# Kernel tuning notes

Hardware: AMD Instinct MI355X
Metric: run time of the kernel (lower is better)

## Reference

```python
import jax, jax.numpy as jnp
import numpy as np

VOXEL_SIZE = 0.05  # init kwarg


def setup_inputs() -> dict:
    key = jax.random.key(0)
    N, B = 4_194_304, 16
    # coords uniform in [0, 5)^3 -> ~100^3 voxel cells per scene at voxel_size=0.05
    coord = jax.random.uniform(key, (N, 3), dtype=jnp.float32) * 5.0
    # cumulative batch offsets (equal-sized scenes), as pointops expects
    offset = (jnp.arange(1, B + 1, dtype=jnp.int32) * (N // B)).astype(jnp.int32)
    return {"coord": coord, "offset": offset}


def _voxel_mean(coord, offset, voxel_size):
    """Faithful jax port of voxelize_helper + segment_csr(mean) + batch2offset.

    Returns:
      n_p    [N,3]  voxel-mean coords, padded with zeros beyond n_voxels
      n_o    [B]    cumulative voxel counts per batch (batch2offset)
      counts [N]    points per voxel (idx_ptr = concat([0], cumsum(counts[valid])))
    """
    N = coord.shape[0]
    B = offset.shape[0]
    # batch id per point from cumulative offsets
    batch = jnp.searchsorted(offset, jnp.arange(N), side='right')  # [N]
    # start = per-batch min coord (start=None path of voxelize_helper)
    start = jax.ops.segment_min(coord, batch, num_segments=B)      # [B,3]
    grid = jnp.floor((coord - start[batch]) / voxel_size).astype(jnp.int32)  # [N,3]
    G = jnp.max(grid) + 1  # grid extent (per-axis upper bound)
    # linearized cluster key: unique per (batch, gx, gy, gz)
    ckey = ((batch * G + grid[:, 0]) * G + grid[:, 1]) * G + grid[:, 2]
    fill = B * G * G * G  # sentinel beyond any real key
    # sorted unique cluster keys == CSR segment order after sorting cluster indices
    uniq, inv = jnp.unique(ckey, return_inverse=True, size=N, fill_value=fill)
    # fused gather + segment-mean (equivalent to coord[sorted_idx] -> segment_csr mean)
    seg_sum = jax.ops.segment_sum(coord, inv, num_segments=N)                 # [N,3]
    counts = jax.ops.segment_sum(jnp.ones((N,), coord.dtype), inv, num_segments=N)
    n_p = seg_sum / jnp.maximum(counts, 1.0)[:, None]
    # batch id per voxel -> batch2offset (cumulative voxel counts)
    valid = uniq < fill
    vbatch = jnp.where(valid, uniq // (G * G * G), B)
    per_batch = jax.ops.segment_sum(valid.astype(jnp.int32), vbatch, num_segments=B + 1)[:B]
    n_o = jnp.cumsum(per_batch)
    return n_p, n_o, counts.astype(jnp.int32)


def reference(coord, offset):
    return _voxel_mean(coord, offset, VOXEL_SIZE)
```

## Files before the change

### kernel.cpp

```cpp
#include <hip/hip_runtime.h>
#include <stdint.h>


typedef unsigned int uint;
typedef unsigned long long u64;

#define VS 0.05f
#define QSCALE (4096.0f / VS)
#define QINV  (VS / 4096.0f)
#define NBUCKET 2048
#define NBLK_P 256
#define DENSE_MAX 4096

__device__ __forceinline__ uint f2m(float f) {
    uint b = __float_as_uint(f);
    return (b & 0x80000000u) ? ~b : (b | 0x80000000u);
}
__device__ __forceinline__ float m2f(uint m) {
    uint b = (m & 0x80000000u) ? (m & 0x7fffffffu) : ~m;
    return __uint_as_float(b);
}

__global__ void k_init(uint* start_m, int B3) {
    int i = blockIdx.x * blockDim.x + threadIdx.x;
    if (i < B3) start_m[i] = 0xFFFFFFFFu;
}

__global__ void __launch_bounds__(256)
k_minmax(const float* __restrict__ coord, const int* __restrict__ offset,
         int N, int B, uint* start_m) {
    __shared__ uint smin[768];
    __shared__ int soff[256];
    int t = threadIdx.x;
    int nb3 = B * 3;
    for (int j = t; j < B; j += 256) soff[j] = offset[j];
    for (int j = t; j < nb3; j += 256) smin[j] = 0xFFFFFFFFu;
    __syncthreads();

    int F = 3 * N;
    int NQ = F >> 2;
    int per = (NQ + gridDim.x - 1) / gridDim.x;
    int qlo = blockIdx.x * per;
    int qhi = min(NQ, qlo + per);
    const float4* __restrict__ c4 = reinterpret_cast<const float4*>(coord);

    bool fast = false;
    int bU = 0;
    if (qlo < qhi) {
        int pF = (4 * qlo) / 3;
        int pL = (4 * qhi - 1) / 3;
        int bF = 0, bL = 0;
        for (int j = 0; j < B; ++j) {
            bF += (pF >= soff[j]) ? 1 : 0;
            bL += (pL >= soff[j]) ? 1 : 0;
        }
        fast = (bF == bL);
        bU = bF;
    }

    if (fast) {
        int q = qlo + t;
        int p0 = q % 3;
        float s0 = INFINITY, s1 = INFINITY, s2 = INFINITY;
        for (;;) {
            if (q >= qhi) break;
            float4 v = c4[q];
            s0 = fminf(s0, fminf(v.x, v.w)); s1 = fminf(s1, v.y); s2 = fminf(s2, v.z);
            q += 256;
            if (q >= qhi) break;
            v = c4[q];
            s1 = fminf(s1, fminf(v.x, v.w)); s2 = fminf(s2, v.y); s0 = fminf(s0, v.z);
            q += 256;
            if (q >= qhi) break;
            v = c4[q];
            s2 = fminf(s2, fminf(v.x, v.w)); s0 = fminf(s0, v.y); s1 = fminf(s1, v.z);
            q += 256;
        }
        float ax, ay, az;
        if (p0 == 0)      { ax = s0; ay = s1; az = s2; }
        else if (p0 == 1) { ax = s2; ay = s0; az = s1; }
        else              { ax = s1; ay = s2; az = s0; }
        for (int d = 32; d; d >>= 1) {
            ax = fminf(ax, __shfl_xor(ax, d));
            ay = fminf(ay, __shfl_xor(ay, d));
            az = fminf(az, __shfl_xor(az, d));
        }
        if ((t & 63) == 0 && ax < INFINITY) {
            atomicMin(&smin[bU * 3 + 0], f2m(ax));
            atomicMin(&smin[bU * 3 + 1], f2m(ay));
            atomicMin(&smin[bU * 3 + 2], f2m(az));
        }
    } else {
        for (int q = qlo + t; q < qhi; q += 256) {
            float4 v = c4[q];
            int e = 4 * q;
            float vals[4] = {v.x, v.y, v.z, v.w};
#pragma unroll
            for (int k = 0; k < 4; ++k) {
                int ee = e + k;
                int pt = ee / 3;
                int axis = ee - 3 * pt;
                int b = 0;
                for (int j = 0; j < B; ++j) b += (pt >= soff[j]) ? 1 : 0;
                atomicMin(&smin[b * 3 + axis], f2m(vals[k]));
            }
        }
    }

    if (blockIdx.x == 0) {
        for (int ee = 4 * NQ + t; ee < F; ee += 256) {
            int pt = ee / 3;
            int axis = ee - 3 * pt;
            int b = 0;
            for (int j = 0; j < B; ++j) b += (pt >= soff[j]) ? 1 : 0;
            atomicMin(&smin[b * 3 + axis], f2m(coord[ee]));
        }
    }
    __syncthreads();
    for (int j = t; j < nb3; j += 256) {
        uint mn = smin[j];
        if (mn != 0xFFFFFFFFu) atomicMin(&start_m[j], mn);
    }
}


__device__ __forceinline__ u64 mk_rec(float x, float y, float z,
                                      float sx, float sy, float sz,
                                      int b, uint& q) {
    int gx = min((int)floorf((x - sx) / VS), 127);
    int gy = min((int)floorf((y - sy) / VS), 127);
    int gz = min((int)floorf((z - sz) / VS), 127);
    float fx = fmaxf(x - (sx + (float)gx * VS), 0.0f);
    float fy = fmaxf(y - (sy + (float)gy * VS), 0.0f);
    float fz = fmaxf(z - (sz + (float)gz * VS), 0.0f);
    uint ux = min((uint)(fx * QSCALE + 0.5f), 4095u);
    uint uy = min((uint)(fy * QSCALE + 0.5f), 4095u);
    uint uz = min((uint)(fz * QSCALE + 0.5f), 4095u);
    uint cell = ((uint)gy << 7) | (uint)gz;
    q = ((uint)b << 7) | (uint)gx;
    return ((u64)q << 50) | ((u64)cell << 36) | ((u64)ux << 24) | ((u64)uy << 12) | (u64)uz;
}

__device__ __forceinline__ void count_point(float x, float y, float z, int b,
                                            float sx, float sy, float sz, int pid,
                                            uint* hist, u64* __restrict__ tmp) {
    uint q;
    u64 rec = mk_rec(x, y, z, sx, sy, sz, b, q);
    atomicAdd(&hist[q], 1u);
    tmp[pid] = rec;
}

__global__ void __launch_bounds__(1024)
k_count3(const float* __restrict__ coord, const int* __restrict__ offset,
         int N, int B, const uint* __restrict__ start_m, uint* __restrict__ histm,
         u64* __restrict__ tmp) {
    __shared__ uint hist[NBUCKET];
    __shared__ int soff[16];
    __shared__ float sstart[48];
    int t = threadIdx.x;
    if (t < B) soff[t] = offset[t];
    if (t < B * 3) sstart[t] = m2f(start_m[t]);
    for (int j = t; j < NBUCKET; j += 1024) hist[j] = 0;
    __syncthreads();
    int chunk = (N + gridDim.x - 1) / gridDim.x;
    int lo = blockIdx.x * chunk, hi = min(N, lo + chunk);
    int bLo = 0, bHi = 0;
    for (int j = 0; j < B; ++j) {
        bLo += (lo >= soff[j]) ? 1 : 0;
        bHi += (hi - 1 >= soff[j]) ? 1 : 0;
    }
    if (lo < hi && bLo == bHi && (lo & 3) == 0) {
        int b = bLo;
        float sx = sstart[b * 3 + 0], sy = sstart[b * 3 + 1], sz = sstart[b * 3 + 2];
        const float4* __restrict__ c4 = reinterpret_cast<const float4*>(coord);
        int gEnd = hi >> 2;
        for (int g = (lo >> 2) + t; g < gEnd; g += 1024) {
            float4 v0 = c4[3 * g], v1 = c4[3 * g + 1], v2 = c4[3 * g + 2];
            int p = 4 * g;
            count_point(v0.x, v0.y, v0.z, b, sx, sy, sz, p + 0, hist, tmp);
            count_point(v0.w, v1.x, v1.y, b, sx, sy, sz, p + 1, hist, tmp);
            count_point(v1.z, v1.w, v2.x, b, sx, sy, sz, p + 2, hist, tmp);
            count_point(v2.y, v2.z, v2.w, b, sx, sy, sz, p + 3, hist, tmp);
        }
        for (int i = (gEnd << 2) + t; i < hi; i += 1024) {
            float x = coord[3 * i + 0], y = coord[3 * i + 1], z = coord[3 * i + 2];
            count_point(x, y, z, b, sx, sy, sz, i, hist, tmp);
        }
    } else {
        for (int i = lo + t; i < hi; i += 1024) {
            float x = coord[3 * i + 0], y = coord[3 * i + 1], z = coord[3 * i + 2];
            int b = 0;
            for (int j = 0; j < B; ++j) b += (i >= soff[j]) ? 1 : 0;
            count_point(x, y, z, b, sstart[b * 3 + 0], sstart[b * 3 + 1],
                        sstart[b * 3 + 2], i, hist, tmp);
        }
    }
    __syncthreads();
    for (int j = t; j < NBUCKET; j += 1024)
        histm[(size_t)j * NBLK_P + blockIdx.x] = hist[j];
}

__global__ void __launch_bounds__(256)
k_scanrow(uint* __restrict__ histm, uint* __restrict__ tot) {
    __shared__ uint wtot[4], woff[4];
    uint* row = histm + (size_t)blockIdx.x * NBLK_P;
    int t = threadIdx.x;
    uint v = row[t];
    uint sc = v;
    for (int d = 1; d < 64; d <<= 1) {
        uint nb = __shfl_up(sc, d, 64);
        if ((t & 63) >= d) sc += nb;
    }
    if ((t & 63) == 63) wtot[t >> 6] = sc;
    __syncthreads();
    if (t == 0) {
        uint r = 0;
#pragma unroll
        for (int k = 0; k < 4; ++k) { woff[k] = r; r += wtot[k]; }
    }
    __syncthreads();
    uint incl = sc + woff[t >> 6];
    row[t] = incl - v;
    if (t == 255) tot[blockIdx.x] = incl;
}

__global__ void __launch_bounds__(1024)
k_scan2048(const uint* __restrict__ in, uint* __restrict__ out) {
    __shared__ uint wtot[16], woff[16];
    int t = threadIdx.x;
    uint a = in[2 * t], bb = in[2 * t + 1];
    uint s = a + bb;
    uint sc = s;
    for (int d = 1; d < 64; d <<= 1) {
        uint nb = __shfl_up(sc, d, 64);
        if ((t & 63) >= d) sc += nb;
    }
    if ((t & 63) == 63) wtot[t >> 6] = sc;
    __syncthreads();
    if (t == 0) {
        uint r = 0;
#pragma unroll
        for (int k = 0; k < 16; ++k) { woff[k] = r; r += wtot[k]; }
    }
    __syncthreads();
    uint incl = sc + woff[t >> 6];
    uint ex = incl - s;
    out[2 * t] = ex;
    out[2 * t + 1] = ex + a;
    if (t == 1023) out[2048] = incl;
}

__global__ void __launch_bounds__(1024)
k_scan2048b(const uint* __restrict__ in, uint* __restrict__ out,
            int B, float* __restrict__ no_out) {
    __shared__ uint wtot[16], woff[16];
    int t = threadIdx.x;
    uint a = in[2 * t], bb = in[2 * t + 1];
    uint s = a + bb;
    uint sc = s;
    for (int d = 1; d < 64; d <<= 1) {
        uint nb = __shfl_up(sc, d, 64);
        if ((t & 63) >= d) sc += nb;
    }
    if ((t & 63) == 63) wtot[t >> 6] = sc;
    __syncthreads();
    if (t == 0) {
        uint r = 0;
#pragma unroll
        for (int k = 0; k < 16; ++k) { woff[k] = r; r += wtot[k]; }
    }
    __syncthreads();
    uint incl = sc + woff[t >> 6];
    uint ex = incl - s;
    out[2 * t] = ex;
    out[2 * t + 1] = ex + a;
    if (t == 1023) out[2048] = incl;
    int tp = t + 1;
    if ((tp & 63) == 0) {
        int b = (tp >> 6) - 1;
        if (b < B) no_out[b] = (float)incl;
    }
}

__global__ void __launch_bounds__(1024)
k_scatter(const u64* __restrict__ tmp, int N,
          const uint* __restrict__ histm, const uint* __restrict__ bucket_base,
          u64* __restrict__ recs) {
    __shared__ uint cursor[NBUCKET];
    int t = threadIdx.x;
    for (int j = t; j < NBUCKET; j += 1024)
        cursor[j] = bucket_base[j] + histm[(size_t)j * NBLK_P + blockIdx.x];
    __syncthreads();
    int chunk = (N + gridDim.x - 1) / gridDim.x;
    int lo = blockIdx.x * chunk, hi = min(N, lo + chunk);
    for (int i = lo + t; i < hi; i += 1024) {
        u64 r = tmp[i];
        uint q = (uint)(r >> 50);
        uint slot = atomicAdd(&cursor[q], 1u);
        recs[slot] = r;
    }
}

__global__ void k_vox(const u64* __restrict__ recs, const uint* __restrict__ bucket_base,
                      uint* __restrict__ voxcount, uint* __restrict__ gmask) {
    __shared__ uint bits[512];
    __shared__ uint wsum[4];
    int q = blockIdx.x;
    uint lo = bucket_base[q], hi = bucket_base[q + 1];
    for (int j = threadIdx.x; j < 512; j += blockDim.x) bits[j] = 0;
    __syncthreads();
    for (uint i = lo + threadIdx.x; i < hi; i += blockDim.x) {
        uint c = (uint)(recs[i] >> 36) & 0x3FFFu;
        atomicOr(&bits[c >> 5], 1u << (c & 31));
    }
    __syncthreads();
    uint s = 0;
    for (int w = threadIdx.x; w < 512; w += blockDim.x) {
        uint m = bits[w];
        gmask[(size_t)q * 512 + w] = m;
        s += __popc(m);
    }
    for (int d = 32; d; d >>= 1) s += __shfl_xor(s, d);
    if ((threadIdx.x & 63) == 0) wsum[threadIdx.x >> 6] = s;
    __syncthreads();
    if (threadIdx.x == 0) voxcount[q] = wsum[0] + wsum[1] + wsum[2] + wsum[3];
}

__global__ void __launch_bounds__(512)
k_emit2(const u64* __restrict__ recs, const uint* __restrict__ bucket_base,
        const uint* __restrict__ voxscan, const uint* __restrict__ gmask,
        const uint* __restrict__ start_m, int N, int B, int out_total,
        float* __restrict__ np_out, float* __restrict__ cnt_out,
        float* __restrict__ out) {
    int t = threadIdx.x;
    if (blockIdx.x >= NBUCKET) {
        uint total = voxscan[NBUCKET];
        int zb = blockIdx.x - NBUCKET;
        int stride = (gridDim.x - NBUCKET) * 512;
        int tid = zb * 512 + t;
        for (int j = 3 * (int)total + tid; j < 3 * N; j += stride) np_out[j] = 0.0f;
        for (int j = (int)total + tid; j < N; j += stride) cnt_out[j] = 0.0f;
        for (int j = 4 * N + B + tid; j < out_total; j += stride) out[j] = 0.0f;
        return;
    }
    __shared__ u64 dense[DENSE_MAX];
    __shared__ uint mask[512], wrank[512];
    __shared__ uint wtot[8], woff[9];
    __shared__ float sstart[48];
    int q = blockIdx.x;
    uint lo = bucket_base[q], hi = bucket_base[q + 1];
    if (lo == hi) return;
    if (t < 48) sstart[t] = m2f(start_m[t]);
    uint m = gmask[(size_t)q * 512 + t];
    mask[t] = m;
    uint c = __popc(m);
    uint sc = c;
    for (int d = 1; d < 64; d <<= 1) {
        uint nb = __shfl_up(sc, d, 64);
        if ((t & 63) >= d) sc += nb;
    }
    if ((t & 63) == 63) wtot[t >> 6] = sc;
    __syncthreads();
    if (t == 0) {
        uint r = 0;
#pragma unroll
        for (int k = 0; k < 8; ++k) { woff[k] = r; r += wtot[k]; }
        woff[8] = r;
    }
    __syncthreads();
    wrank[t] = sc - c + woff[t >> 6];
    uint vc = woff[8];
    uint base_r = voxscan[q];
    int b = q >> 7, gx = q & 127;
    float cx = sstart[b * 3 + 0] + (float)gx * VS;
    float sy = sstart[b * 3 + 1], sz = sstart[b * 3 + 2];
    bool single = (vc <= (uint)DENSE_MAX);
    for (uint segbase = 0; segbase < vc; segbase += DENSE_MAX) {
        uint seglen = min(vc - segbase, (uint)DENSE_MAX);
        for (uint j = t; j < seglen; j += 512) dense[j] = 0ull;
        __syncthreads();
        if (single) {
            for (uint i = lo + t; i < hi; i += 512) {
                u64 rec = recs[i];
                uint cc = (uint)(rec >> 36) & 0x3FFFu;
                uint w = cc >> 5, bit = cc & 31;
                uint r = wrank[w] + __popc(mask[w] & ((1u << bit) - 1u));
                u64 enc = (((rec >> 24) & 0xFFFull) << 46) | (((rec >> 12) & 0xFFFull) << 28)
                        | ((rec & 0xFFFull) << 10) | 1ull;
                atomicAdd(&dense[r], enc);
            }
        } else {
            for (uint i = lo + t; i < hi; i += 512) {
                u64 rec = recs[i];
                uint cc = (uint)(rec >> 36) & 0x3FFFu;
                uint w = cc >> 5, bit = cc & 31;
                uint r = wrank[w] + __popc(mask[w] & ((1u << bit) - 1u));
                if (r >= segbase && r < segbase + seglen) {
                    u64 enc = (((rec >> 24) & 0xFFFull) << 46) | (((rec >> 12) & 0xFFFull) << 28)
                            | ((rec & 0xFFFull) << 10) | 1ull;
                    atomicAdd(&dense[r - segbase], enc);
                }
            }
        }
        __syncthreads();
        {
            uint mm = mask[t];
            uint r = wrank[t];
            uint kbase = (uint)t << 5;
            while (mm) {
                uint bit = (uint)__ffs(mm) - 1u;
                mm &= mm - 1u;
                if (r >= segbase && r < segbase + seglen) {
                    uint cell = kbase + bit;
                    uint gy = cell >> 7, gz = cell & 127u;
                    u64 p = dense[r - segbase];
                    float cnt = (float)(uint)(p & 1023ull);
                    float inv = 1.0f / fmaxf(cnt, 1.0f);
                    uint uz = (uint)((p >> 10) & 0x3FFFFull);
                    uint uy = (uint)((p >> 28) & 0x3FFFFull);
                    uint ux = (uint)(p >> 46);
                    uint r_out = base_r + r;
                    np_out[3 * r_out + 0] = cx + ((float)ux * QINV) * inv;
                    np_out[3 * r_out + 1] = sy + (float)gy * VS + ((float)uy * QINV) * inv;
                    np_out[3 * r_out + 2] = sz + (float)gz * VS + ((float)uz * QINV) * inv;
                    cnt_out[r_out] = cnt;
                }
                ++r;
            }
        }
        __syncthreads();
    }
}


__device__ __forceinline__ void point_grid(const float* __restrict__ coord, int i,
                                           const int* soff, const float* sstart, int B,
                                           float& x, float& y, float& z,
                                           int& b, int& gx, int& gy, int& gz) {
    x = coord[3 * i + 0]; y = coord[3 * i + 1]; z = coord[3 * i + 2];
    b = 0;
    for (int j = 0; j < B; ++j) b += (i >= soff[j]) ? 1 : 0;
    gx = min((int)floorf((x - sstart[b * 3 + 0]) / VS), 127);
    gy = min((int)floorf((y - sstart[b * 3 + 1]) / VS), 127);
    gz = min((int)floorf((z - sstart[b * 3 + 2]) / VS), 127);
}

__device__ __forceinline__ u64 frac12(float x, float y, float z,
                                      const float* sstart, int b,
                                      int gx, int gy, int gz) {
    float fx = fmaxf(x - (sstart[b * 3 + 0] + (float)gx * VS), 0.0f);
    float fy = fmaxf(y - (sstart[b * 3 + 1] + (float)gy * VS), 0.0f);
    float fz = fmaxf(z - (sstart[b * 3 + 2] + (float)gz * VS), 0.0f);
    uint ux = min((uint)(fx * QSCALE + 0.5f), 4095u);
    uint uy = min((uint)(fy * QSCALE + 0.5f), 4095u);
    uint uz = min((uint)(fz * QSCALE + 0.5f), 4095u);
    return ((u64)ux << 24) | ((u64)uy << 12) | (u64)uz;
}

__global__ void k_hist(const float* __restrict__ coord, const int* __restrict__ offset,
                       int N, int B, const uint* __restrict__ start_m,
                       uint* __restrict__ mask) {
    __shared__ int soff[256];
    __shared__ float sstart[768];
    for (int j = threadIdx.x; j < B; j += blockDim.x) soff[j] = offset[j];
    for (int j = threadIdx.x; j < B * 3; j += blockDim.x) sstart[j] = m2f(start_m[j]);
    __syncthreads();
    int i = blockIdx.x * blockDim.x + threadIdx.x;
    if (i >= N) return;
    float x, y, z; int b, gx, gy, gz;
    point_grid(coord, i, soff, sstart, B, x, y, z, b, gx, gy, gz);
    uint key = ((uint)b << 21) | ((uint)gx << 14) | ((uint)gy << 7) | (uint)gz;
    atomicOr(&mask[key >> 5], 1u << (key & 31));
}

__global__ void k_scan1(const uint* __restrict__ mask, uint* __restrict__ partial) {
    int base = blockIdx.x * 1024 + threadIdx.x * 4;
    uint4 m = *(const uint4*)(mask + base);
    uint s = __popc(m.x) + __popc(m.y) + __popc(m.z) + __popc(m.w);
    for (int d = 32; d; d >>= 1) s += __shfl_xor(s, d);
    __shared__ uint wsum[4];
    if ((threadIdx.x & 63) == 0) wsum[threadIdx.x >> 6] = s;
    __syncthreads();
    if (threadIdx.x == 0) partial[blockIdx.x] = wsum[0] + wsum[1] + wsum[2] + wsum[3];
}

__global__ void k_scan2(uint* partial, int P, uint* total) {
    __shared__ uint t[256];
    uint carry = 0;
    for (int base = 0; base < P; base += 256) {
        int j = base + threadIdx.x;
        uint v = (j < P) ? partial[j] : 0;
        t[threadIdx.x] = v;
        __syncthreads();
        for (int d = 1; d < 256; d <<= 1) {
            uint add = (threadIdx.x >= d) ? t[threadIdx.x - d] : 0;
            __syncthreads();
            t[threadIdx.x] += add;
            __syncthreads();
        }
        uint inc = t[threadIdx.x];
        uint chunk = t[255];
        if (j < P) partial[j] = carry + inc - v;
        __syncthreads();
        carry += chunk;
    }
    if (threadIdx.x == 0) *total = carry;
}

__global__ void k_scan3(const uint* __restrict__ mask, const uint* __restrict__ partial,
                        uint* __restrict__ wordrank) {
    int base = blockIdx.x * 1024 + threadIdx.x * 4;
    uint4 m = *(const uint4*)(mask + base);
    uint c0 = __popc(m.x), c1 = __popc(m.y), c2 = __popc(m.z), c3 = __popc(m.w);
    uint s = c0 + c1 + c2 + c3;
    __shared__ uint t[256];
    t[threadIdx.x] = s;
    __syncthreads();
    for (int d = 1; d < 256; d <<= 1) {
        uint add = (threadIdx.x >= d) ? t[threadIdx.x - d] : 0;
        __syncthreads();
        t[threadIdx.x] += add;
        __syncthreads();
    }
    uint ex = t[threadIdx.x] - s + partial[blockIdx.x];
    uint4 r;
    r.x = ex; r.y = ex + c0; r.z = ex + c0 + c1; r.w = ex + c0 + c1 + c2;
    *(uint4*)(wordrank + base) = r;
}

__global__ void k_no(const uint* mask, const uint* wordrank, const uint* total,
                     float* no_out, int B, int W) {
    int b = blockIdx.x * blockDim.x + threadIdx.x;
    if (b >= B) return;
    long long idx = (long long)(b + 1) << 21;
    uint w = (uint)(idx >> 5);
    uint v;
    if (w >= (uint)W) v = *total;
    else v = wordrank[w];
    no_out[b] = (float)v;
}

__global__ void k_accum_sparse(const float* __restrict__ coord, const int* __restrict__ offset,
                               int N, int B, const uint* __restrict__ start_m,
                               const uint* __restrict__ mask, const uint* __restrict__ wordrank,
                               u64* __restrict__ packed) {
    __shared__ int soff[256];
    __shared__ float sstart[768];
    for (int j = threadIdx.x; j < B; j += blockDim.x) soff[j] = offset[j];
    for (int j = threadIdx.x; j < B * 3; j += blockDim.x) sstart[j] = m2f(start_m[j]);
    __syncthreads();
    int i = blockIdx.x * blockDim.x + threadIdx.x;
    if (i >= N) return;
    float x, y, z; int b, gx, gy, gz;
    point_grid(coord, i, soff, sstart, B, x, y, z, b, gx, gy, gz);
    uint key = ((uint)b << 21) | ((uint)gx << 14) | ((uint)gy << 7) | (uint)gz;
    uint w = key >> 5, bit = key & 31;
    uint r = wordrank[w] + __popc(mask[w] & ((1u << bit) - 1u));
    u64 f = frac12(x, y, z, sstart, b, gx, gy, gz);
    u64 enc = (((f >> 24) & 0xFFFull) << 46) | (((f >> 12) & 0xFFFull) << 28)
            | ((f & 0xFFFull) << 10) | 1ull;
    atomicAdd(&packed[r], enc);
}

__global__ void k_decode_sparse(const uint* __restrict__ mask, const uint* __restrict__ wordrank,
                                const uint* __restrict__ start_m,
                                const u64* __restrict__ packed, int W,
                                float* __restrict__ np_out, float* __restrict__ cnt_out) {
    __shared__ float sstart[48];
    for (int j = threadIdx.x; j < 48; j += blockDim.x) sstart[j] = m2f(start_m[j]);
    __syncthreads();
    int w = blockIdx.x * blockDim.x + threadIdx.x;
    if (w >= W) return;
    uint m = mask[w];
    if (m == 0) return;
    uint r = wordrank[w];
    uint kbase = (uint)w << 5;
    while (m) {
        uint bit = (uint)__ffs(m) - 1u;
        m &= m - 1u;
        uint key = kbase + bit;
        u64 p = packed[r];
        float cnt = (float)(uint)(p & 1023ull);
        float inv = 1.0f / fmaxf(cnt, 1.0f);
        uint uz = (uint)((p >> 10) & 0x3FFFFull);
        uint uy = (uint)((p >> 28) & 0x3FFFFull);
        uint ux = (uint)(p >> 46);
        uint b = key >> 21;
        uint gx = (key >> 14) & 127u;
        uint gy = (key >> 7) & 127u;
        uint gz = key & 127u;
        np_out[3 * r + 0] = sstart[b * 3 + 0] + (float)gx * VS + ((float)ux * QINV) * inv;
        np_out[3 * r + 1] = sstart[b * 3 + 1] + (float)gy * VS + ((float)uy * QINV) * inv;
        np_out[3 * r + 2] = sstart[b * 3 + 2] + (float)gz * VS + ((float)uz * QINV) * inv;
        cnt_out[r] = cnt;
        ++r;
    }
}

extern "C" void kernel_launch(void* const* d_in, const int* in_sizes, int n_in,
                              void* d_out, int out_size, void* d_ws, size_t ws_size,
                              hipStream_t stream) {
    const float* coord = (const float*)d_in[0];
    const int* offset = (const int*)d_in[1];
    int N = in_sizes[0] / 3;
    int B = in_sizes[1];

    float* out = (float*)d_out;
    float* np_out = out;
    float* no_out = out + (size_t)3 * N;
    float* cnt_out = no_out + B;

    uint8_t* base = (uint8_t*)d_ws;
    uint* start_m = (uint*)base;
    uint* total = start_m + (size_t)B * 3;

    uintptr_t p = (uintptr_t)(total + 1);
    p = (p + 255) & ~(uintptr_t)255;
    uint* histm = (uint*)p;          p += (size_t)NBUCKET * NBLK_P * 4;
    p = (p + 255) & ~(uintptr_t)255;
    uint* tot = (uint*)p;            p += (size_t)NBUCKET * 4;
    p = (p + 255) & ~(uintptr_t)255;
    uint* bucket_base = (uint*)p;    p += (size_t)(NBUCKET + 1) * 4;
    p = (p + 255) & ~(uintptr_t)255;
    uint* voxcount = (uint*)p;       p += (size_t)NBUCKET * 4;
    p = (p + 255) & ~(uintptr_t)255;
    uint* voxscan = (uint*)p;        p += (size_t)(NBUCKET + 1) * 4;
    p = (p + 255) & ~(uintptr_t)255;
    uint* gmask = (uint*)p;          p += (size_t)NBUCKET * 512 * 4;
    p = (p + 255) & ~(uintptr_t)255;
    u64* recs = (u64*)p;             p += (size_t)N * 8;
    p = (p + 255) & ~(uintptr_t)255;
    u64* tmp = (u64*)p;              p += (size_t)N * 8;
    size_t need_part = p - (uintptr_t)base;

    k_init<<<(B * 3 + 255) / 256, 256, 0, stream>>>(start_m, B * 3);
    k_minmax<<<2048, 256, 0, stream>>>(coord, offset, N, B, start_m);

    if (B <= 16 && ws_size >= need_part) {
        k_count3<<<NBLK_P, 1024, 0, stream>>>(coord, offset, N, B, start_m, histm, tmp);
        k_scanrow<<<NBUCKET, 256, 0, stream>>>(histm, tot);
        k_scan2048<<<1, 1024, 0, stream>>>(tot, bucket_base);
        k_scatter<<<NBLK_P, 1024, 0, stream>>>(tmp, N, histm, bucket_base, recs);
        k_vox<<<NBUCKET, 256, 0, stream>>>(recs, bucket_base, voxcount, gmask);
        k_scan2048b<<<1, 1024, 0, stream>>>(voxcount, voxscan, B, no_out);
        k_emit2<<<NBUCKET + 1024, 512, 0, stream>>>(recs, bucket_base, voxscan, gmask,
                                                    start_m, N, B, out_size,
                                                    np_out, cnt_out, out);
    } else {
        hipMemsetAsync(d_out, 0, (size_t)out_size * sizeof(float), stream);
        size_t W = (size_t)B << 16;
        int nblk1 = (int)(W / 1024);
        uintptr_t sp = (uintptr_t)(total + 1);
        sp = (sp + 255) & ~(uintptr_t)255;
        uint* partial = (uint*)sp;   sp += (size_t)nblk1 * 4;
        sp = (sp + 255) & ~(uintptr_t)255;
        uint* mask = (uint*)sp;      sp += W * 4;
        sp = (sp + 255) & ~(uintptr_t)255;
        uint* wordrank = (uint*)sp;  sp += W * 4;
        sp = (sp + 255) & ~(uintptr_t)255;
        u64* packed = (u64*)sp;
        int nb = (N + 255) / 256;
        hipMemsetAsync(mask, 0, W * sizeof(uint), stream);
        hipMemsetAsync(packed, 0, (size_t)N * sizeof(u64), stream);
        k_hist<<<nb, 256, 0, stream>>>(coord, offset, N, B, start_m, mask);
        k_scan1<<<nblk1, 256, 0, stream>>>(mask, partial);
        k_scan2<<<1, 256, 0, stream>>>(partial, nblk1, total);
        k_scan3<<<nblk1, 256, 0, stream>>>(mask, partial, wordrank);
        k_no<<<(B + 63) / 64, 64, 0, stream>>>(mask, wordrank, total, no_out, B, (int)W);
        k_accum_sparse<<<nb, 256, 0, stream>>>(coord, offset, N, B, start_m, mask,
                                               wordrank, packed);
        k_decode_sparse<<<(int)((W + 255) / 256), 256, 0, stream>>>(mask, wordrank, start_m,
                                                                    packed, (int)W,
                                                                    np_out, cnt_out);
    }
}
```

Before: 237.9 us.

## Widen emit kernel to 1024 threads and emit voxels via rank-indexed cell table

The emit kernel now runs 1024 threads per bucket. Before accumulation, each mask-word thread records the cell index for each voxel rank in a shared u16 table. Output is then written by iterating ranks contiguously across all threads, instead of having each mask-word thread walk its own bits serially. The aim is to remove the serial, divergent per-word output loop and to get coalesced output writes. The cost is extra shared memory and a larger block, which may reduce occupancy. k_vox is also simplified to fixed 256-thread indexing.

Measured after the change: 194.1 us (median of 2 runs). 1.23x faster.

```diff
diff --git a/kernel.cpp b/kernel.cpp
--- a/kernel.cpp
+++ b/kernel.cpp
@@ -3,6 +3,7 @@
 
 
 typedef unsigned int uint;
+typedef unsigned short u16;
 typedef unsigned long long u64;
 
 #define VS 0.05f
@@ -301,32 +302,33 @@
     }
 }
 
-__global__ void k_vox(const u64* __restrict__ recs, const uint* __restrict__ bucket_base,
-                      uint* __restrict__ voxcount, uint* __restrict__ gmask) {
+__global__ void __launch_bounds__(256)
+k_vox(const u64* __restrict__ recs, const uint* __restrict__ bucket_base,
+      uint* __restrict__ voxcount, uint* __restrict__ gmask) {
     __shared__ uint bits[512];
     __shared__ uint wsum[4];
     int q = blockIdx.x;
+    int t = threadIdx.x;
     uint lo = bucket_base[q], hi = bucket_base[q + 1];
-    for (int j = threadIdx.x; j < 512; j += blockDim.x) bits[j] = 0;
-    __syncthreads();
-    for (uint i = lo + threadIdx.x; i < hi; i += blockDim.x) {
+    bits[t] = 0;
+    bits[t + 256] = 0;
+    __syncthreads();
+    for (uint i = lo + t; i < hi; i += 256) {
         uint c = (uint)(recs[i] >> 36) & 0x3FFFu;
         atomicOr(&bits[c >> 5], 1u << (c & 31));
     }
     __syncthreads();
-    uint s = 0;
-    for (int w = threadIdx.x; w < 512; w += blockDim.x) {
-        uint m = bits[w];
-        gmask[(size_t)q * 512 + w] = m;
-        s += __popc(m);
-    }
+    uint m0 = bits[t], m1 = bits[t + 256];
+    gmask[(size_t)q * 512 + t] = m0;
+    gmask[(size_t)q * 512 + t + 256] = m1;
+    uint s = __popc(m0) + __popc(m1);
     for (int d = 32; d; d >>= 1) s += __shfl_xor(s, d);
-    if ((threadIdx.x & 63) == 0) wsum[threadIdx.x >> 6] = s;
-    __syncthreads();
-    if (threadIdx.x == 0) voxcount[q] = wsum[0] + wsum[1] + wsum[2] + wsum[3];
-}
-
-__global__ void __launch_bounds__(512)
+    if ((t & 63) == 0) wsum[t >> 6] = s;
+    __syncthreads();
+    if (t == 0) voxcount[q] = wsum[0] + wsum[1] + wsum[2] + wsum[3];
+}
+
+__global__ void __launch_bounds__(1024)
 k_emit2(const u64* __restrict__ recs, const uint* __restrict__ bucket_base,
         const uint* __restrict__ voxscan, const uint* __restrict__ gmask,
         const uint* __restrict__ start_m, int N, int B, int out_total,
@@ -336,8 +338,8 @@
     if (blockIdx.x >= NBUCKET) {
         uint total = voxscan[NBUCKET];
         int zb = blockIdx.x - NBUCKET;
-        int stride = (gridDim.x - NBUCKET) * 512;
-        int tid = zb * 512 + t;
+        int stride = (gridDim.x - NBUCKET) * 1024;
+        int tid = zb * 1024 + t;
         for (int j = 3 * (int)total + tid; j < 3 * N; j += stride) np_out[j] = 0.0f;
         for (int j = (int)total + tid; j < N; j += stride) cnt_out[j] = 0.0f;
         for (int j = 4 * N + B + tid; j < out_total; j += stride) out[j] = 0.0f;
@@ -345,88 +347,81 @@
     }
     __shared__ u64 dense[DENSE_MAX];
     __shared__ uint mask[512], wrank[512];
+    __shared__ u16 cellOf[DENSE_MAX];
     __shared__ uint wtot[8], woff[9];
     __shared__ float sstart[48];
     int q = blockIdx.x;
     uint lo = bucket_base[q], hi = bucket_base[q + 1];
     if (lo == hi) return;
     if (t < 48) sstart[t] = m2f(start_m[t]);
-    uint m = gmask[(size_t)q * 512 + t];
-    mask[t] = m;
-    uint c = __popc(m);
+    uint m = 0, c = 0;
+    if (t < 512) {
+        m = gmask[(size_t)q * 512 + t];
+        mask[t] = m;
+        c = __popc(m);
+    }
     uint sc = c;
     for (int d = 1; d < 64; d <<= 1) {
         uint nb = __shfl_up(sc, d, 64);
         if ((t & 63) >= d) sc += nb;
     }
-    if ((t & 63) == 63) wtot[t >> 6] = sc;
+    if (t < 512 && (t & 63) == 63) wtot[t >> 6] = sc;
     __syncthreads();
     if (t == 0) {
         uint r = 0;
-#pragma unroll
         for (int k = 0; k < 8; ++k) { woff[k] = r; r += wtot[k]; }
         woff[8] = r;
     }
     __syncthreads();
-    wrank[t] = sc - c + woff[t >> 6];
+    uint myrank = sc - c + ((t < 512) ? woff[t >> 6] : 0);
+    if (t < 512) wrank[t] = myrank;
     uint vc = woff[8];
     uint base_r = voxscan[q];
     int b = q >> 7, gx = q & 127;
     float cx = sstart[b * 3 + 0] + (float)gx * VS;
     float sy = sstart[b * 3 + 1], sz = sstart[b * 3 + 2];
-    bool single = (vc <= (uint)DENSE_MAX);
     for (uint segbase = 0; segbase < vc; segbase += DENSE_MAX) {
         uint seglen = min(vc - segbase, (uint)DENSE_MAX);
-        for (uint j = t; j < seglen; j += 512) dense[j] = 0ull;
-        __syncthreads();
-        if (single) {
-            for (uint i = lo + t; i < hi; i += 512) {
-                u64 rec = recs[i];
-                uint cc = (uint)(rec >> 36) & 0x3FFFu;
-                uint w = cc >> 5, bit = cc & 31;
-                uint r = wrank[w] + __popc(mask[w] & ((1u << bit) - 1u));
-                u64 enc = (((rec >> 24) & 0xFFFull) << 46) | (((rec >> 12) & 0xFFFull) << 28)
-                        | ((rec & 0xFFFull) << 10) | 1ull;
-                atomicAdd(&dense[r], enc);
-            }
-        } else {
-            for (uint i = lo + t; i < hi; i += 512) {
-                u64 rec = recs[i];
-                uint cc = (uint)(rec >> 36) & 0x3FFFu;
-                uint w = cc >> 5, bit = cc & 31;
-                uint r = wrank[w] + __popc(mask[w] & ((1u << bit) - 1u));
-                if (r >= segbase && r < segbase + seglen) {
-                    u64 enc = (((rec >> 24) & 0xFFFull) << 46) | (((rec >> 12) & 0xFFFull) << 28)
-                            | ((rec & 0xFFFull) << 10) | 1ull;
-                    atomicAdd(&dense[r - segbase], enc);
-                }
-            }
-        }
-        __syncthreads();
-        {
-            uint mm = mask[t];
-            uint r = wrank[t];
+        for (uint j = t; j < seglen; j += 1024) dense[j] = 0ull;
+        if (t < 512) {
+            uint mm = m;
+            uint r = myrank;
             uint kbase = (uint)t << 5;
             while (mm) {
                 uint bit = (uint)__ffs(mm) - 1u;
                 mm &= mm - 1u;
-                if (r >= segbase && r < segbase + seglen) {
-                    uint cell = kbase + bit;
-                    uint gy = cell >> 7, gz = cell & 127u;
-                    u64 p = dense[r - segbase];
-                    float cnt = (float)(uint)(p & 1023ull);
-                    float inv = 1.0f / fmaxf(cnt, 1.0f);
-                    uint uz = (uint)((p >> 10) & 0x3FFFFull);
-                    uint uy = (uint)((p >> 28) & 0x3FFFFull);
-                    uint ux = (uint)(p >> 46);
-                    uint r_out = base_r + r;
-                    np_out[3 * r_out + 0] = cx + ((float)ux * QINV) * inv;
-                    np_out[3 * r_out + 1] = sy + (float)gy * VS + ((float)uy * QINV) * inv;
-                    np_out[3 * r_out + 2] = sz + (float)gz * VS + ((float)uz * QINV) * inv;
-                    cnt_out[r_out] = cnt;
-                }
+                if (r >= segbase && r < segbase + seglen)
+                    cellOf[r - segbase] = (u16)(kbase + bit);
                 ++r;
             }
+        }
+        __syncthreads();
+        for (uint i = lo + t; i < hi; i += 1024) {
+            u64 rec = recs[i];
+            uint cc = (uint)(rec >> 36) & 0x3FFFu;
+            uint w = cc >> 5, bit = cc & 31;
+            uint r = wrank[w] + __popc(mask[w] & ((1u << bit) - 1u));
+            if (r >= segbase && r < segbase + seglen) {
+                u64 enc = (((rec >> 24) & 0xFFFull) << 46) | (((rec >> 12) & 0xFFFull) << 28)
+                        | ((rec & 0xFFFull) << 10) | 1ull;
+                atomicAdd(&dense[r - segbase], enc);
+            }
+        }
+        __syncthreads();
+        for (uint rr = segbase + t; rr < segbase + seglen; rr += 1024) {
+            uint cell = cellOf[rr - segbase];
+            uint gy = cell >> 7, gz = cell & 127u;
+            u64 p = dense[rr - segbase];
+            float cnt = (float)(uint)(p & 1023ull);
+            float inv = 1.0f / fmaxf(cnt, 1.0f);
+            uint uz = (uint)((p >> 10) & 0x3FFFFull);
+            uint uy = (uint)((p >> 28) & 0x3FFFFull);
+            uint ux = (uint)(p >> 46);
+            uint r_out = base_r + rr;
+            np_out[3 * r_out + 0] = cx + ((float)ux * QINV) * inv;
+            np_out[3 * r_out + 1] = sy + (float)gy * VS + ((float)uy * QINV) * inv;
+            np_out[3 * r_out + 2] = sz + (float)gz * VS + ((float)uz * QINV) * inv;
+            cnt_out[r_out] = cnt;
         }
         __syncthreads();
     }
@@ -643,9 +638,9 @@
         k_scatter<<<NBLK_P, 1024, 0, stream>>>(tmp, N, histm, bucket_base, recs);
         k_vox<<<NBUCKET, 256, 0, stream>>>(recs, bucket_base, voxcount, gmask);
         k_scan2048b<<<1, 1024, 0, stream>>>(voxcount, voxscan, B, no_out);
-        k_emit2<<<NBUCKET + 1024, 512, 0, stream>>>(recs, bucket_base, voxscan, gmask,
-                                                    start_m, N, B, out_size,
-                                                    np_out, cnt_out, out);
+        k_emit2<<<NBUCKET + 1024, 1024, 0, stream>>>(recs, bucket_base, voxscan, gmask,
+                                                     start_m, N, B, out_size,
+                                                     np_out, cnt_out, out);
     } else {
         hipMemsetAsync(d_out, 0, (size_t)out_size * sizeof(float), stream);
         size_t W = (size_t)B << 16;
```
